# Performance work log

Measured on AMD Instinct MI355X. Metric: run time of the kernel, lower is better.

Reference implementation:

```python
import jax, jax.numpy as jnp
import numpy as np

NUM_CLASSES = 90
ALPHA = 0.5
GAMMA = 2.0
EPS = 1e-4


def _calc_iou(a, b):
    # a: [A,4] anchors in (y1,x1,y2,x2); b: [M,4] gt boxes in (x1,y1,x2,y2)
    area = (b[:, 2] - b[:, 0]) * (b[:, 3] - b[:, 1])  # [M]
    iw = jnp.minimum(a[:, 3, None], b[None, :, 2]) - jnp.maximum(a[:, 1, None], b[None, :, 0])
    ih = jnp.minimum(a[:, 2, None], b[None, :, 3]) - jnp.maximum(a[:, 0, None], b[None, :, 1])
    iw = jnp.clip(iw, 0.0)
    ih = jnp.clip(ih, 0.0)
    ua = ((a[:, 2] - a[:, 0]) * (a[:, 3] - a[:, 1]))[:, None] + area[None, :] - iw * ih
    ua = jnp.clip(ua, 1e-8)
    return (iw * ih) / ua  # [A,M]


def _per_image_loss(cls, reg, ann, anchor, anchor_w, anchor_h, anchor_cx, anchor_cy):
    # cls: [A,C]; reg: [A,4]; ann: [M,5]
    valid = ann[:, 4] != -1.0  # [M]
    p = jnp.clip(cls, EPS, 1.0 - EPS)
    iou = _calc_iou(anchor, ann[:, :4])
    iou = jnp.where(valid[None, :], iou, -1.0)
    iou_max = jnp.max(iou, axis=1)              # [A]
    iou_argmax = jnp.argmax(iou, axis=1)        # [A]

    pos = iou_max >= 0.5                         # [A]
    num_pos = jnp.sum(pos)
    base = jnp.where((iou_max < 0.4) | pos, 0.0, -1.0)[:, None]  # [A,1]
    assigned = ann[iou_argmax]                   # [A,5]
    lbl = assigned[:, 4].astype(jnp.int32)
    onehot = (jnp.arange(NUM_CLASSES)[None, :] == lbl[:, None]) & pos[:, None]
    targets = jnp.where(onehot, 1.0, base)       # [A,C] in {-1,0,1}

    # focal BCE
    is_one = targets == 1.0
    alpha_factor = jnp.where(is_one, ALPHA, 1.0 - ALPHA)
    focal_w = alpha_factor * jnp.where(is_one, 1.0 - p, p) ** GAMMA
    bce = -(targets * jnp.log(p) + (1.0 - targets) * jnp.log(1.0 - p))
    cls_loss = jnp.where(targets != -1.0, focal_w * bce, 0.0)
    npos_f = num_pos.astype(p.dtype)
    cls_l = jnp.sum(cls_loss) / jnp.maximum(npos_f, 1.0)

    gt_w = assigned[:, 2] - assigned[:, 0]
    gt_h = assigned[:, 3] - assigned[:, 1]
    gt_cx = assigned[:, 0] + 0.5 * gt_w
    gt_cy = assigned[:, 1] + 0.5 * gt_h
    gt_w = jnp.clip(gt_w, 1.0)
    gt_h = jnp.clip(gt_h, 1.0)
    t_dx = (gt_cx - anchor_cx) / anchor_w
    t_dy = (gt_cy - anchor_cy) / anchor_h
    t_dw = jnp.log(gt_w / anchor_w)
    t_dh = jnp.log(gt_h / anchor_h)
    t = jnp.stack((t_dy, t_dx, t_dh, t_dw), axis=1)  # [A,4]
    diff = jnp.abs(t - reg)
    rl = jnp.where(diff <= 1.0 / 9.0, 0.5 * 9.0 * diff * diff, diff - 0.5 / 9.0)
    rl = jnp.where(pos[:, None], rl, 0.0)
    reg_l = jnp.where(num_pos > 0,
                      jnp.sum(rl) / jnp.maximum(npos_f * 4.0, 1.0),
                      jnp.zeros((), p.dtype))
    return cls_l, reg_l


def reference(classifications, regressions, anchors, annotations):
    anchor = anchors[0]  # [A,4] (y1,x1,y2,x2)
    aw = anchor[:, 3] - anchor[:, 1]
    ah = anchor[:, 2] - anchor[:, 0]
    acx = anchor[:, 1] + 0.5 * aw
    acy = anchor[:, 0] + 0.5 * ah
    cls_l, reg_l = jax.vmap(
        lambda c, r, a: _per_image_loss(c, r, a, anchor, aw, ah, acx, acy)
    )(classifications, regressions, annotations)
    # mode='mean'
    return (jnp.mean(cls_l, keepdims=True), jnp.mean(reg_l, keepdims=True))


def setup_inputs() -> dict:
    key = jax.random.key(0)
    k1, k2, k3, k4, k5, k6, k7 = jax.random.split(key, 7)
    B, A, C, M = 8, 49104, 90, 32
    classifications = jax.random.uniform(k1, (B, A, C), jnp.float32, 0.001, 0.999)
    regressions = jax.random.normal(k2, (B, A, 4), jnp.float32)
    # anchors in (y1,x1,y2,x2)
    ctr = jax.random.uniform(k3, (A, 2), jnp.float32, 16.0, 496.0)  # (cy,cx)
    wh = jax.random.uniform(k4, (A, 2), jnp.float32, 16.0, 128.0)   # (h,w)
    anchor = jnp.concatenate([ctr - 0.5 * wh, ctr + 0.5 * wh], axis=1)  # y1,x1,y2,x2
    anchors = anchor[None]  # [1,A,4]
    # annotations in (x1,y1,x2,y2,label), all valid
    gctr = jax.random.uniform(k5, (B, M, 2), jnp.float32, 64.0, 448.0)  # (cx,cy)
    gwh = jax.random.uniform(k6, (B, M, 2), jnp.float32, 32.0, 160.0)   # (w,h)
    boxes = jnp.concatenate([gctr - 0.5 * gwh, gctr + 0.5 * gwh], axis=2)
    labels = jax.random.randint(k7, (B, M, 1), 0, C).astype(jnp.float32)
    annotations = jnp.concatenate([boxes, labels], axis=2)
    return {"classifications": classifications, "regressions": regressions,
            "anchors": anchors, "annotations": annotations}
```

## Files before the change

kernel.cpp:

```cpp
#include <hip/hip_runtime.h>
#include <hip/hip_bf16.h>
#include <stdint.h>

#define NB 8
#define NA 49104
#define NC 90
#define NM 32
#define FEPS 1e-4f
#define CHUNKS_IMG (NA * NC / 4)
#define LN2_HALF 0.34657359027997264f
#define CPT 8
#define FBLK ((CHUNKS_IMG + 256 * CPT - 1) / (256 * CPT))

typedef float f32x4 __attribute__((ext_vector_type(4)));


__global__ __launch_bounds__(256) void fl_assign(
    const float* __restrict__ anchors,
    const float* __restrict__ regressions,
    const float* __restrict__ annotations,
    double* __restrict__ reg_sum,
    int* __restrict__ npos,
    uint32_t* __restrict__ meta)
{
    const int b = blockIdx.y;
    const int a = blockIdx.x * 256 + threadIdx.x;

    __shared__ float s_ann[NM * 5];
    if (threadIdx.x < NM * 5)
        s_ann[threadIdx.x] = annotations[b * NM * 5 + threadIdx.x];
    __syncthreads();

    float rsum = 0.0f;
    int pcnt = 0;

    if (a < NA) {
        const f32x4 av = ((const f32x4*)anchors)[a];
        const float ay1 = av.x, ax1 = av.y, ay2 = av.z, ax2 = av.w;
        const float aw = ax2 - ax1, ah = ay2 - ay1;
        const float aarea = aw * ah;

        float best = -2.0f;
        int bm = 0;
        #pragma unroll 4
        for (int m = 0; m < NM; ++m) {
            const float bx1 = s_ann[m * 5 + 0];
            const float by1 = s_ann[m * 5 + 1];
            const float bx2 = s_ann[m * 5 + 2];
            const float by2 = s_ann[m * 5 + 3];
            const float lab = s_ann[m * 5 + 4];
            const float area = (bx2 - bx1) * (by2 - by1);
            float iw = fminf(ax2, bx2) - fmaxf(ax1, bx1);
            float ih = fminf(ay2, by2) - fmaxf(ay1, by1);
            iw = fmaxf(iw, 0.0f);
            ih = fmaxf(ih, 0.0f);
            const float inter = iw * ih;
            const float ua = fmaxf(aarea + area - inter, 1e-8f);
            float iou = inter / ua;
            if (lab == -1.0f) iou = -1.0f;
            if (iou > best) { best = iou; bm = m; }
        }

        const bool pos = best >= 0.5f;
        const bool bz = (best < 0.4f) || pos;
        const int lbl = ((int)s_ann[bm * 5 + 4]) & 0x7f;
        meta[b * NA + a] = (uint32_t)lbl | (pos ? 0x80u : 0u) | (bz ? 0x100u : 0u);

        if (pos) {
            pcnt = 1;
            const float bx1 = s_ann[bm * 5 + 0];
            const float by1 = s_ann[bm * 5 + 1];
            const float bx2 = s_ann[bm * 5 + 2];
            const float by2 = s_ann[bm * 5 + 3];
            float gw = bx2 - bx1, gh = by2 - by1;
            const float gcx = bx1 + 0.5f * gw;
            const float gcy = by1 + 0.5f * gh;
            gw = fmaxf(gw, 1.0f);
            gh = fmaxf(gh, 1.0f);
            const float acx = ax1 + 0.5f * aw;
            const float acy = ay1 + 0.5f * ah;

            const f32x4 rv = ((const f32x4*)regressions)[(size_t)b * NA + a];
            const float t0 = (gcy - acy) / ah;
            const float t1 = (gcx - acx) / aw;
            const float t2 = logf(gh / ah);
            const float t3 = logf(gw / aw);

            float d;
            d = fabsf(t0 - rv.x); rsum += (d <= 1.0f/9.0f) ? 4.5f*d*d : d - 1.0f/18.0f;
            d = fabsf(t1 - rv.y); rsum += (d <= 1.0f/9.0f) ? 4.5f*d*d : d - 1.0f/18.0f;
            d = fabsf(t2 - rv.z); rsum += (d <= 1.0f/9.0f) ? 4.5f*d*d : d - 1.0f/18.0f;
            d = fabsf(t3 - rv.w); rsum += (d <= 1.0f/9.0f) ? 4.5f*d*d : d - 1.0f/18.0f;
        }
    }

    #pragma unroll
    for (int off = 32; off > 0; off >>= 1) {
        rsum += __shfl_down(rsum, off);
        pcnt += __shfl_down(pcnt, off);
    }
    __shared__ float s_r[4];
    __shared__ int s_p[4];
    const int wave = threadIdx.x >> 6;
    if ((threadIdx.x & 63) == 0) { s_r[wave] = rsum; s_p[wave] = pcnt; }
    __syncthreads();
    if (threadIdx.x == 0) {
        const float r = s_r[0] + s_r[1] + s_r[2] + s_r[3];
        const int p = s_p[0] + s_p[1] + s_p[2] + s_p[3];
        if (p) atomicAdd(&npos[b], p);
        if (r != 0.0f) atomicAdd(&reg_sum[b], (double)r);
    }
}

__global__ __launch_bounds__(256) void fl_focal(
    const f32x4* __restrict__ cls,
    const uint32_t* __restrict__ meta,
    double* __restrict__ cls_sum)
{
    const int b = blockIdx.y;
    const f32x4* cb = cls + (size_t)b * CHUNKS_IMG;
    const uint32_t* mb = meta + b * NA;

    const int i0 = blockIdx.x * (256 * CPT) + threadIdx.x;

    f32x4 v[CPT];
    int   ic[CPT];
    float okf[CPT];
    #pragma unroll
    for (int u = 0; u < CPT; ++u) {
        const int i = i0 + u * 256;
        const bool ok = i < CHUNKS_IMG;
        okf[u] = ok ? 1.0f : 0.0f;
        ic[u] = ok ? i : (CHUNKS_IMG - 1);
        v[u] = __builtin_nontemporal_load(&cb[ic[u]]);
    }

    int   c0[CPT], tA[CPT], tB[CPT];
    float wA[CPT], wB[CPT];
    #pragma unroll
    for (int u = 0; u < CPT; ++u) {
        const uint32_t e0 = (uint32_t)ic[u] * 4u;
        const uint32_t aid = e0 / 90u;
        c0[u] = (int)(e0 - aid * 90u);
        const uint32_t m0 = mb[aid];
        const uint32_t m1 = mb[aid + 1];
        wA[u] = ((m0 & 0x100u) ? 1.0f : 0.0f) * okf[u];
        wB[u] = ((m1 & 0x100u) ? 1.0f : 0.0f) * okf[u];
        tA[u] = (m0 & 0x80u) ? (int)(m0 & 0x7fu) : 0x7fff;
        tB[u] = ((m1 & 0x80u) ? (int)(m1 & 0x7fu) : 0x7fff) + 90;
    }

    float acc = 0.0f;
    #pragma unroll
    for (int u = 0; u < CPT; ++u) {
        const float pv[4] = {v[u].x, v[u].y, v[u].z, v[u].w};
        #pragma unroll
        for (int j = 0; j < 4; ++j) {
            const int cc = c0[u] + j;
            const bool inA = cc < 90;
            const float w = inA ? wA[u] : wB[u];
            const int tgt = inA ? tA[u] : tB[u];
            float p = fminf(fmaxf(pv[j], FEPS), 1.0f - FEPS);
            const float pf = (cc == tgt) ? 1.0f - p : p;
            const float l = __log2f(1.0f - pf);
            acc = fmaf(pf * pf * l, w, acc);
        }
    }

    #pragma unroll
    for (int off = 32; off > 0; off >>= 1)
        acc += __shfl_down(acc, off);
    __shared__ float s_r[4];
    const int wave = threadIdx.x >> 6;
    if ((threadIdx.x & 63) == 0) s_r[wave] = acc;
    __syncthreads();
    if (threadIdx.x == 0) {
        const float r = s_r[0] + s_r[1] + s_r[2] + s_r[3];
        atomicAdd(&cls_sum[b], (double)r * -(double)LN2_HALF);
    }
}

__global__ void fl_final(
    const double* __restrict__ reg_sum,
    const double* __restrict__ cls_sum,
    const int* __restrict__ npos,
    float* __restrict__ out)
{
    if (threadIdx.x == 0) {
        double cl = 0.0, rl = 0.0;
        for (int b = 0; b < NB; ++b) {
            const int np = npos[b];
            const double d = (double)(np > 1 ? np : 1);
            cl += cls_sum[b] / d;
            if (np > 0) rl += reg_sum[b] / (4.0 * (double)np);
        }
        out[0] = (float)(cl / (double)NB);
        out[1] = (float)(rl / (double)NB);
    }
}

extern "C" void kernel_launch(void* const* d_in, const int* in_sizes, int n_in,
                              void* d_out, int out_size, void* d_ws, size_t ws_size,
                              hipStream_t stream) {
    const float* cls = (const float*)d_in[0];
    const float* reg = (const float*)d_in[1];
    const float* anc = (const float*)d_in[2];
    const float* ann = (const float*)d_in[3];
    float* out = (float*)d_out;

    char* ws = (char*)d_ws;
    double*   reg_sum = (double*)(ws + 0);
    double*   cls_sum = (double*)(ws + 64);
    int*      npos    = (int*)(ws + 128);
    uint32_t* meta    = (uint32_t*)(ws + 256);

    (void)hipMemsetAsync(d_ws, 0, 256, stream);

    dim3 ga((NA + 255) / 256, NB);
    fl_assign<<<ga, 256, 0, stream>>>(anc, reg, ann, reg_sum, npos, meta);
    dim3 gf(FBLK, NB);
    fl_focal<<<gf, 256, 0, stream>>>((const f32x4*)cls, meta, cls_sum);
    fl_final<<<1, 64, 0, stream>>>(reg_sum, cls_sum, npos, out);
}
```

Before: 260.9 us.

## Fuse anchor assignment and focal loss into one kernel with per-block partials

Merges the anchor-assignment and focal-loss kernels so each block computes assignment for its 256 anchors into shared memory, then streams the matching classification slice. This removes the global metadata write/read, the memset, and the double atomics, which are replaced by per-block partial sums reduced in a parallel final kernel. The trade is that each block serializes IoU work before its streaming loads, and a larger per-block unrolled load set may raise register pressure.

```diff
diff --git a/kernel.cpp b/kernel.cpp
--- a/kernel.cpp
+++ b/kernel.cpp
@@ -1,5 +1,4 @@
 #include <hip/hip_runtime.h>
-#include <hip/hip_bf16.h>
 #include <stdint.h>
 
 #define NB 8
@@ -7,32 +6,84 @@
 #define NC 90
 #define NM 32
 #define FEPS 1e-4f
+#define APB 256
+#define GX ((NA + APB - 1) / APB)
+#define CPB (APB * NC / 4)
 #define CHUNKS_IMG (NA * NC / 4)
-#define LN2_HALF 0.34657359027997264f
-#define CPT 8
-#define FBLK ((CHUNKS_IMG + 256 * CPT - 1) / (256 * CPT))
+#define LN2_HALF 0.34657359027997264
 
 typedef float f32x4 __attribute__((ext_vector_type(4)));
 
 
-__global__ __launch_bounds__(256) void fl_assign(
+template<int N>
+__device__ inline float focal_group(const f32x4* __restrict__ ci, int gbase,
+                                    int cstart, int t,
+                                    const float* s_w, const int* s_t)
+{
+    f32x4 v[N];
+    int   cl[N];
+    float vf[N];
+    #pragma unroll
+    for (int u = 0; u < N; ++u) {
+        const int c = cstart + u * 256 + t;
+        vf[u] = (c < CPB) ? 1.0f : 0.0f;
+        cl[u] = (c < CPB) ? c : (CPB - 1);
+        int ic = gbase + cl[u];
+        ic = (ic < CHUNKS_IMG) ? ic : (CHUNKS_IMG - 1);
+        v[u] = ci[ic];
+    }
+    float acc = 0.0f;
+    #pragma unroll
+    for (int u = 0; u < N; ++u) {
+        const int e0   = cl[u] * 4;
+        const int aidl = (e0 * 46604) >> 22;
+        const int c0   = e0 - aidl * 90;
+        const float w0 = s_w[aidl]     * vf[u];
+        const float w1 = s_w[aidl + 1] * vf[u];
+        const int   t0 = s_t[aidl];
+        const int   t1 = s_t[aidl + 1] + 90;
+        const float pv[4] = {v[u].x, v[u].y, v[u].z, v[u].w};
+        #pragma unroll
+        for (int j = 0; j < 4; ++j) {
+            const int cc  = c0 + j;
+            const bool inA = cc < 90;
+            const float w  = inA ? w0 : w1;
+            const int  tgt = inA ? t0 : t1;
+            float p = fminf(fmaxf(pv[j], FEPS), 1.0f - FEPS);
+            const float pf = (cc == tgt) ? 1.0f - p : p;
+            const float l  = __log2f(1.0f - pf);
+            acc = fmaf(pf * pf * l, w, acc);
+        }
+    }
+    return acc;
+}
+
+__global__ __launch_bounds__(256) void fl_fused(
     const float* __restrict__ anchors,
+    const f32x4* __restrict__ cls,
     const float* __restrict__ regressions,
     const float* __restrict__ annotations,
-    double* __restrict__ reg_sum,
-    int* __restrict__ npos,
-    uint32_t* __restrict__ meta)
+    float* __restrict__ cls_p,
+    float* __restrict__ reg_p,
+    int* __restrict__ np_p)
 {
-    const int b = blockIdx.y;
-    const int a = blockIdx.x * 256 + threadIdx.x;
+    const int bx = blockIdx.x;
+    const int b  = blockIdx.y;
+    const int t  = threadIdx.x;
 
     __shared__ float s_ann[NM * 5];
-    if (threadIdx.x < NM * 5)
-        s_ann[threadIdx.x] = annotations[b * NM * 5 + threadIdx.x];
-    __syncthreads();
-
+    __shared__ float s_w[APB + 1];
+    __shared__ int   s_t[APB + 1];
+
+    if (t < NM * 5)
+        s_ann[t] = annotations[b * NM * 5 + t];
+    __syncthreads();
+
+    const int a = bx * APB + t;
     float rsum = 0.0f;
-    int pcnt = 0;
+    int   pcnt = 0;
+    float wv = 0.0f;
+    int   tv = 0x7fff;
 
     if (a < NA) {
         const f32x4 av = ((const f32x4*)anchors)[a];
@@ -62,9 +113,9 @@
         }
 
         const bool pos = best >= 0.5f;
-        const bool bz = (best < 0.4f) || pos;
-        const int lbl = ((int)s_ann[bm * 5 + 4]) & 0x7f;
-        meta[b * NA + a] = (uint32_t)lbl | (pos ? 0x80u : 0u) | (bz ? 0x100u : 0u);
+        const bool bz  = (best < 0.4f) || pos;
+        wv = bz ? 1.0f : 0.0f;
+        tv = pos ? (((int)s_ann[bm * 5 + 4]) & 0x7f) : 0x7fff;
 
         if (pos) {
             pcnt = 1;
@@ -94,105 +145,72 @@
         }
     }
 
-    #pragma unroll
-    for (int off = 32; off > 0; off >>= 1) {
+    s_w[t] = wv;
+    s_t[t] = tv;
+    if (t == 0) { s_w[APB] = 0.0f; s_t[APB] = 0x7fff; }
+    __syncthreads();
+
+    const f32x4* ci = cls + (size_t)b * CHUNKS_IMG;
+    const int gbase = bx * CPB;
+
+    float acc;
+    acc  = focal_group<8>(ci, gbase, 0,    t, s_w, s_t);
+    acc += focal_group<8>(ci, gbase, 2048, t, s_w, s_t);
+    acc += focal_group<7>(ci, gbase, 4096, t, s_w, s_t);
+
+    #pragma unroll
+    for (int off = 32; off; off >>= 1) {
+        acc  += __shfl_down(acc, off);
         rsum += __shfl_down(rsum, off);
         pcnt += __shfl_down(pcnt, off);
     }
-    __shared__ float s_r[4];
-    __shared__ int s_p[4];
-    const int wave = threadIdx.x >> 6;
-    if ((threadIdx.x & 63) == 0) { s_r[wave] = rsum; s_p[wave] = pcnt; }
-    __syncthreads();
-    if (threadIdx.x == 0) {
-        const float r = s_r[0] + s_r[1] + s_r[2] + s_r[3];
-        const int p = s_p[0] + s_p[1] + s_p[2] + s_p[3];
-        if (p) atomicAdd(&npos[b], p);
-        if (r != 0.0f) atomicAdd(&reg_sum[b], (double)r);
-    }
-}
-
-__global__ __launch_bounds__(256) void fl_focal(
-    const f32x4* __restrict__ cls,
-    const uint32_t* __restrict__ meta,
-    double* __restrict__ cls_sum)
-{
-    const int b = blockIdx.y;
-    const f32x4* cb = cls + (size_t)b * CHUNKS_IMG;
-    const uint32_t* mb = meta + b * NA;
-
-    const int i0 = blockIdx.x * (256 * CPT) + threadIdx.x;
-
-    f32x4 v[CPT];
-    int   ic[CPT];
-    float okf[CPT];
-    #pragma unroll
-    for (int u = 0; u < CPT; ++u) {
-        const int i = i0 + u * 256;
-        const bool ok = i < CHUNKS_IMG;
-        okf[u] = ok ? 1.0f : 0.0f;
-        ic[u] = ok ? i : (CHUNKS_IMG - 1);
-        v[u] = __builtin_nontemporal_load(&cb[ic[u]]);
-    }
-
-    int   c0[CPT], tA[CPT], tB[CPT];
-    float wA[CPT], wB[CPT];
-    #pragma unroll
-    for (int u = 0; u < CPT; ++u) {
-        const uint32_t e0 = (uint32_t)ic[u] * 4u;
-        const uint32_t aid = e0 / 90u;
-        c0[u] = (int)(e0 - aid * 90u);
-        const uint32_t m0 = mb[aid];
-        const uint32_t m1 = mb[aid + 1];
-        wA[u] = ((m0 & 0x100u) ? 1.0f : 0.0f) * okf[u];
-        wB[u] = ((m1 & 0x100u) ? 1.0f : 0.0f) * okf[u];
-        tA[u] = (m0 & 0x80u) ? (int)(m0 & 0x7fu) : 0x7fff;
-        tB[u] = ((m1 & 0x80u) ? (int)(m1 & 0x7fu) : 0x7fff) + 90;
-    }
-
-    float acc = 0.0f;
-    #pragma unroll
-    for (int u = 0; u < CPT; ++u) {
-        const float pv[4] = {v[u].x, v[u].y, v[u].z, v[u].w};
-        #pragma unroll
-        for (int j = 0; j < 4; ++j) {
-            const int cc = c0[u] + j;
-            const bool inA = cc < 90;
-            const float w = inA ? wA[u] : wB[u];
-            const int tgt = inA ? tA[u] : tB[u];
-            float p = fminf(fmaxf(pv[j], FEPS), 1.0f - FEPS);
-            const float pf = (cc == tgt) ? 1.0f - p : p;
-            const float l = __log2f(1.0f - pf);
-            acc = fmaf(pf * pf * l, w, acc);
-        }
-    }
-
-    #pragma unroll
-    for (int off = 32; off > 0; off >>= 1)
-        acc += __shfl_down(acc, off);
-    __shared__ float s_r[4];
-    const int wave = threadIdx.x >> 6;
-    if ((threadIdx.x & 63) == 0) s_r[wave] = acc;
-    __syncthreads();
-    if (threadIdx.x == 0) {
-        const float r = s_r[0] + s_r[1] + s_r[2] + s_r[3];
-        atomicAdd(&cls_sum[b], (double)r * -(double)LN2_HALF);
-    }
-}
-
-__global__ void fl_final(
-    const double* __restrict__ reg_sum,
-    const double* __restrict__ cls_sum,
-    const int* __restrict__ npos,
+    __shared__ float sa[4], sr[4];
+    __shared__ int   sp[4];
+    const int wid = t >> 6;
+    if ((t & 63) == 0) { sa[wid] = acc; sr[wid] = rsum; sp[wid] = pcnt; }
+    __syncthreads();
+    if (t == 0) {
+        const int slot = b * GX + bx;
+        cls_p[slot] = sa[0] + sa[1] + sa[2] + sa[3];
+        reg_p[slot] = sr[0] + sr[1] + sr[2] + sr[3];
+        np_p[slot]  = sp[0] + sp[1] + sp[2] + sp[3];
+    }
+}
+
+__global__ __launch_bounds__(256) void fl_final(
+    const float* __restrict__ cls_p,
+    const float* __restrict__ reg_p,
+    const int* __restrict__ np_p,
     float* __restrict__ out)
 {
-    if (threadIdx.x == 0) {
+    const int t = threadIdx.x;
+    const int img = t >> 5, lane = t & 31;
+
+    float cs = 0.0f, rs = 0.0f;
+    int ns = 0;
+    #pragma unroll
+    for (int k = 0; k < GX / 32; ++k) {
+        const int s = img * GX + k * 32 + lane;
+        cs += cls_p[s];
+        rs += reg_p[s];
+        ns += np_p[s];
+    }
+    #pragma unroll
+    for (int off = 16; off; off >>= 1) {
+        cs += __shfl_down(cs, off);
+        rs += __shfl_down(rs, off);
+        ns += __shfl_down(ns, off);
+    }
+    __shared__ double s_c[8], s_r[8];
+    __shared__ int    s_n[8];
+    if (lane == 0) { s_c[img] = (double)cs; s_r[img] = (double)rs; s_n[img] = ns; }
+    __syncthreads();
+    if (t == 0) {
         double cl = 0.0, rl = 0.0;
         for (int b = 0; b < NB; ++b) {
-            const int np = npos[b];
-            const double d = (double)(np > 1 ? np : 1);
-            cl += cls_sum[b] / d;
-            if (np > 0) rl += reg_sum[b] / (4.0 * (double)np);
+            const int np = s_n[b];
+            cl += s_c[b] * (-LN2_HALF) / (double)(np > 1 ? np : 1);
+            if (np > 0) rl += s_r[b] / (4.0 * (double)np);
         }
         out[0] = (float)(cl / (double)NB);
         out[1] = (float)(rl / (double)NB);
@@ -209,16 +227,12 @@
     float* out = (float*)d_out;
 
     char* ws = (char*)d_ws;
-    double*   reg_sum = (double*)(ws + 0);
-    double*   cls_sum = (double*)(ws + 64);
-    int*      npos    = (int*)(ws + 128);
-    uint32_t* meta    = (uint32_t*)(ws + 256);
-
-    (void)hipMemsetAsync(d_ws, 0, 256, stream);
-
-    dim3 ga((NA + 255) / 256, NB);
-    fl_assign<<<ga, 256, 0, stream>>>(anc, reg, ann, reg_sum, npos, meta);
-    dim3 gf(FBLK, NB);
-    fl_focal<<<gf, 256, 0, stream>>>((const f32x4*)cls, meta, cls_sum);
-    fl_final<<<1, 64, 0, stream>>>(reg_sum, cls_sum, npos, out);
-}
+    float* cls_p = (float*)(ws + 0);
+    float* reg_p = (float*)(ws + 8192);
+    int*   np_p  = (int*)(ws + 16384);
+
+    dim3 g(GX, NB);
+    fl_fused<<<g, 256, 0, stream>>>(anc, (const f32x4*)cls, reg, ann,
+                                    cls_p, reg_p, np_p);
+    fl_final<<<1, 256, 0, stream>>>(cls_p, reg_p, np_p, out);
+}
```

New measurement: 214.4 us. 17.8% less time.
